# Performance work log

Measured on AMD Instinct MI355X. Metric: run time of the kernel, lower is better.

Reference implementation:

```python
import jax, jax.numpy as jnp
import numpy as np

N, H, K, T, B, IN_DIM, L = 1024, 64, 2, 12, 8, 2, 2
NNZ = 16384  # N * avg_degree(16)
M = 2 * K + 1  # supports_len * max_diffusion_step + 1 = 5


def setup_inputs() -> dict:
    key = jax.random.key(0)
    ks = jax.random.split(key, 13)

    def xavier(k, shape):
        std = 1.414 * (2.0 / (shape[0] + shape[1])) ** 0.5
        return std * jax.random.normal(k, shape, dtype=jnp.float32)

    F0 = IN_DIM + H  # 66
    F1 = 2 * H       # 128
    return {
        "inputs": jax.random.normal(ks[0], (T, B, N * IN_DIM), dtype=jnp.float32),
        "initial_hidden_state": jnp.zeros((L, B, N * H), dtype=jnp.float32),
        "support_rows": jax.random.randint(ks[1], (2, NNZ), 0, N, dtype=jnp.int32),
        "support_cols": jax.random.randint(ks[2], (2, NNZ), 0, N, dtype=jnp.int32),
        # scale like a random-walk-normalized adjacency (avg degree ~16)
        "support_vals": jax.random.uniform(ks[3], (2, NNZ), dtype=jnp.float32) / 16.0,
        "Wg0": xavier(ks[4], (F0 * M, 2 * H)),
        "bg0": 0.01 * jax.random.normal(ks[5], (2 * H,), dtype=jnp.float32),
        "Wc0": xavier(ks[6], (F0 * M, H)),
        "bc0": 0.01 * jax.random.normal(ks[7], (H,), dtype=jnp.float32),
        "Wg1": xavier(ks[8], (F1 * M, 2 * H)),
        "bg1": 0.01 * jax.random.normal(ks[9], (2 * H,), dtype=jnp.float32),
        "Wc1": xavier(ks[10], (F1 * M, H)),
        "bc1": 0.01 * jax.random.normal(ks[11], (H,), dtype=jnp.float32),
    }


def reference(inputs, initial_hidden_state, support_rows, support_cols, support_vals,
              Wg0, bg0, Wc0, bc0, Wg1, bg1, Wc1, bc1):
    supports = [(support_rows[i], support_cols[i], support_vals[i])
                for i in range(support_rows.shape[0])]

    def spmm(rows, cols, vals, x):  # sparse [N,N] @ x[N,FB]
        return jax.ops.segment_sum(vals[:, None] * x[cols], rows, num_segments=N)

    def diffuse(x):  # x: [B, N, F] -> [B*N, F*M] (Chebyshev-style recurrence)
        Bz, _, F = x.shape
        x0 = x.transpose(1, 2, 0).reshape(N, F * Bz)
        mats = [x0]
        for rows, cols, vals in supports:
            x1 = spmm(rows, cols, vals, x0)
            mats.append(x1)
            xkm2, xkm1 = x0, x1
            for _ in range(2, K + 1):
                xk = 2.0 * spmm(rows, cols, vals, xkm1) - xkm2
                mats.append(xk)
                xkm2, xkm1 = xkm1, xk
        Xs = jnp.stack(mats, 0).reshape(len(mats), N, F, Bz)
        return Xs.transpose(3, 1, 2, 0).reshape(Bz * N, F * len(mats))

    def cell(params, inp_t, state):  # one DCGRU step
        Wg, bg, Wc, bc = params
        Bz = inp_t.shape[0]
        xi = inp_t.reshape(Bz, N, -1)
        gates = jax.nn.sigmoid(
            diffuse(jnp.concatenate([xi, state.reshape(Bz, N, H)], 2)) @ Wg + bg
        ).reshape(Bz, N, 2 * H)
        r = gates[..., :H].reshape(Bz, N * H)
        u = gates[..., H:].reshape(Bz, N * H)
        cand_in = jnp.concatenate([xi, (r * state).reshape(Bz, N, H)], 2)
        c = jnp.tanh((diffuse(cand_in) @ Wc + bc).reshape(Bz, N * H))
        return u * state + (1.0 - u) * c

    layer_params = [(Wg0, bg0, Wc0, bc0), (Wg1, bg1, Wc1, bc1)]
    cur = inputs  # [T, B, N*input_dim]
    hiddens = []
    for l, params in enumerate(layer_params):
        def step(state, x_t, params=params):
            ns = cell(params, x_t, state)
            return ns, ns
        h_last, outs = jax.lax.scan(step, initial_hidden_state[l], cur)
        hiddens.append(h_last)
        cur = outs  # [T, B, N*H]
    return jnp.stack(hiddens, 0), cur
```

## Files before the change

### kernel.cpp

```cpp
#include <hip/hip_runtime.h>
#include <hip/hip_bf16.h>
#include <math.h>

#define NN 1024
#define HH 64
#define TT 12
#define BB 8
#define INDIM 2
#define LL 2
#define NNZE 16384
#define MM 5

#define FP0 96
#define FP1 128
#define CP0 (BB * FP0)
#define CP1 (BB * FP1)

static constexpr size_t BNH = (size_t)BB * NN * HH;

typedef short bf16x8 __attribute__((ext_vector_type(8)));
typedef float f32x4 __attribute__((ext_vector_type(4)));

__global__ void zero_int_kernel(int* p, int n) {
  int i = blockIdx.x * blockDim.x + threadIdx.x;
  if (i < n) p[i] = 0;
}

__global__ void copy_kernel(const float* __restrict__ src, float* __restrict__ dst, int n) {
  int i = blockIdx.x * blockDim.x + threadIdx.x;
  if (i < n) dst[i] = src[i];
}

__global__ void csr_count_kernel(const int* __restrict__ rows, int* __restrict__ counts) {
  int i = blockIdx.x * blockDim.x + threadIdx.x;
  if (i < 2 * NNZE) {
    int s = i / NNZE;
    atomicAdd(&counts[s * NN + rows[i]], 1);
  }
}

__global__ void csr_scan_kernel(const int* __restrict__ counts, int* __restrict__ row_start,
                                int* __restrict__ cursor) {
  __shared__ int bufA[NN];
  __shared__ int bufB[NN];
  int s = blockIdx.x;
  int t = threadIdx.x;
  bufA[t] = counts[s * NN + t];
  __syncthreads();
  int* src = bufA;
  int* dst = bufB;
  for (int off = 1; off < NN; off <<= 1) {
    dst[t] = src[t] + (t >= off ? src[t - off] : 0);
    __syncthreads();
    int* tmp = src; src = dst; dst = tmp;
  }
  row_start[s * (NN + 1) + t + 1] = src[t];
  cursor[s * NN + t] = (t == 0) ? 0 : src[t - 1];
  if (t == 0) row_start[s * (NN + 1)] = 0;
}

__global__ void csr_scatter_kernel(const int* __restrict__ rows, const int* __restrict__ colsIn,
                                   const float* __restrict__ valsIn, int* __restrict__ cursor,
                                   int* __restrict__ colsOut, float* __restrict__ valsOut) {
  int i = blockIdx.x * blockDim.x + threadIdx.x;
  if (i < 2 * NNZE) {
    int s = i / NNZE;
    int r = rows[i];
    int pos = atomicAdd(&cursor[s * NN + r], 1);
    colsOut[s * NNZE + pos] = colsIn[i];
    valsOut[s * NNZE + pos] = valsIn[i];
  }
}

__global__ void permwT_kernel(const float* __restrict__ W, unsigned short* __restrict__ WTh,
                              unsigned short* __restrict__ WTl, int F, int Fp, int J, int reord) {
  int Ktot = MM * Fp;
  int total = J * Ktot;
  for (int idx = blockIdx.x * blockDim.x + threadIdx.x; idx < total;
       idx += gridDim.x * blockDim.x) {
    int k = idx % Ktot;
    int j = idx / Ktot;
    int m = k / Fp;
    int fn = k - m * Fp;
    int fo;
    if (reord) {
      fo = (fn < HH) ? fn + INDIM : (fn < HH + INDIM ? fn - HH : -1);
    } else {
      fo = (fn < F) ? fn : -1;
    }
    float x = (fo >= 0) ? W[(size_t)(fo * MM + m) * J + j] : 0.f;
    unsigned u = __float_as_uint(x);
    unsigned short h = (unsigned short)(u >> 16);
    float hf = __uint_as_float(u & 0xFFFF0000u);
    WTh[idx] = h;
    WTl[idx] = (unsigned short)(__float_as_uint(x - hf) >> 16);
  }
}

template <int MODE>
__global__ __launch_bounds__(256) void spmm1_l1_kernel(
    const int* __restrict__ row_start, const int* __restrict__ cols,
    const float* __restrict__ vals, const float* __restrict__ xi,
    const float* __restrict__ state,
    const float* __restrict__ gates,
    float* __restrict__ mats) {
  const int r = blockIdx.x, s = blockIdx.y, tid = threadIdx.x;
  const int b = tid >> 5;
  const int f = (tid & 31) * 4;
  const bool isX = (f < HH);
  if (MODE && isX) return;
  const float* src = isX ? xi : state;
  const size_t srcBase = (size_t)b * NN * HH + (isX ? f : f - HH);
  const size_t gBase = (size_t)b * NN * (2 * HH) + (f - HH);

  const int* rs = row_start + s * (NN + 1);
  const int* cs = cols + s * NNZE;
  const float* vs = vals + s * NNZE;
  const int start = rs[r], end = rs[r + 1];

  float4 a0 = {0.f, 0.f, 0.f, 0.f}, a1 = {0.f, 0.f, 0.f, 0.f};
  int e = start;
  for (; e + 1 < end; e += 2) {
    int c0 = cs[e], c1 = cs[e + 1];
    float v0 = vs[e], v1 = vs[e + 1];
    float4 x0 = *(const float4*)(src + srcBase + (size_t)c0 * HH);
    float4 x1 = *(const float4*)(src + srcBase + (size_t)c1 * HH);
    if (MODE && !isX) {
      float4 g0 = *(const float4*)(gates + gBase + (size_t)c0 * (2 * HH));
      float4 g1 = *(const float4*)(gates + gBase + (size_t)c1 * (2 * HH));
      x0.x *= g0.x; x0.y *= g0.y; x0.z *= g0.z; x0.w *= g0.w;
      x1.x *= g1.x; x1.y *= g1.y; x1.z *= g1.z; x1.w *= g1.w;
    }
    a0.x += v0 * x0.x; a0.y += v0 * x0.y; a0.z += v0 * x0.z; a0.w += v0 * x0.w;
    a1.x += v1 * x1.x; a1.y += v1 * x1.y; a1.z += v1 * x1.z; a1.w += v1 * x1.w;
  }
  if (e < end) {
    int c0 = cs[e];
    float v0 = vs[e];
    float4 x0 = *(const float4*)(src + srcBase + (size_t)c0 * HH);
    if (MODE && !isX) {
      float4 g0 = *(const float4*)(gates + gBase + (size_t)c0 * (2 * HH));
      x0.x *= g0.x; x0.y *= g0.y; x0.z *= g0.z; x0.w *= g0.w;
    }
    a0.x += v0 * x0.x; a0.y += v0 * x0.y; a0.z += v0 * x0.z; a0.w += v0 * x0.w;
  }
  float4 o;
  o.x = a0.x + a1.x; o.y = a0.y + a1.y; o.z = a0.z + a1.z; o.w = a0.w + a1.w;
  *(float4*)(mats + (size_t)(1 + 2 * s) * (NN * CP1) + (size_t)r * CP1 + tid * 4) = o;

  if (s == 0) {
    float4 x = *(const float4*)(src + srcBase + (size_t)r * HH);
    if (MODE && !isX) {
      float4 g = *(const float4*)(gates + gBase + (size_t)r * (2 * HH));
      x.x *= g.x; x.y *= g.y; x.z *= g.z; x.w *= g.w;
    }
    *(float4*)(mats + (size_t)r * CP1 + tid * 4) = x;
  }
}

template <int MODE>
__global__ __launch_bounds__(256) void spmm1_l0_kernel(
    const int* __restrict__ row_start, const int* __restrict__ cols,
    const float* __restrict__ vals, const float* __restrict__ xi,
    const float* __restrict__ state,
    const float* __restrict__ gates,
    float* __restrict__ mats) {
  const int tid = threadIdx.x;
  constexpr int SLOTS = FP0 / 4;
  if (tid >= BB * SLOTS) return;
  const int r = blockIdx.x, s = blockIdx.y;
  const int b = tid / SLOTS;
  const int fn = (tid - b * SLOTS) * 4;
  const int c4 = b * FP0 + fn;

  float* x1p = mats + (size_t)(1 + 2 * s) * (NN * CP0) + (size_t)r * CP0 + c4;
  float* x0p = mats + (size_t)r * CP0 + c4;

  const int* rs = row_start + s * (NN + 1);
  const int* cs = cols + s * NNZE;
  const float* vs = vals + s * NNZE;
  const int start = rs[r], end = rs[r + 1];

  if (fn < HH) {
    const float* sb = state + (size_t)b * NN * HH + fn;
    const float* gb = gates + (size_t)b * NN * (2 * HH) + fn;
    float4 a0 = {0.f, 0.f, 0.f, 0.f}, a1 = {0.f, 0.f, 0.f, 0.f};
    int e = start;
    for (; e + 1 < end; e += 2) {
      int c0 = cs[e], c1 = cs[e + 1];
      float v0 = vs[e], v1 = vs[e + 1];
      float4 x0 = *(const float4*)(sb + (size_t)c0 * HH);
      float4 x1 = *(const float4*)(sb + (size_t)c1 * HH);
      if (MODE) {
        float4 g0 = *(const float4*)(gb + (size_t)c0 * (2 * HH));
        float4 g1 = *(const float4*)(gb + (size_t)c1 * (2 * HH));
        x0.x *= g0.x; x0.y *= g0.y; x0.z *= g0.z; x0.w *= g0.w;
        x1.x *= g1.x; x1.y *= g1.y; x1.z *= g1.z; x1.w *= g1.w;
      }
      a0.x += v0 * x0.x; a0.y += v0 * x0.y; a0.z += v0 * x0.z; a0.w += v0 * x0.w;
      a1.x += v1 * x1.x; a1.y += v1 * x1.y; a1.z += v1 * x1.z; a1.w += v1 * x1.w;
    }
    if (e < end) {
      int c0 = cs[e];
      float v0 = vs[e];
      float4 x0 = *(const float4*)(sb + (size_t)c0 * HH);
      if (MODE) {
        float4 g0 = *(const float4*)(gb + (size_t)c0 * (2 * HH));
        x0.x *= g0.x; x0.y *= g0.y; x0.z *= g0.z; x0.w *= g0.w;
      }
      a0.x += v0 * x0.x; a0.y += v0 * x0.y; a0.z += v0 * x0.z; a0.w += v0 * x0.w;
    }
    float4 o;
    o.x = a0.x + a1.x; o.y = a0.y + a1.y; o.z = a0.z + a1.z; o.w = a0.w + a1.w;
    *(float4*)x1p = o;
    if (s == 0) {
      float4 x = *(const float4*)(sb + (size_t)r * HH);
      if (MODE) {
        float4 g = *(const float4*)(gb + (size_t)r * (2 * HH));
        x.x *= g.x; x.y *= g.y; x.z *= g.z; x.w *= g.w;
      }
      *(float4*)x0p = x;
    }
  } else if (fn == HH) {
    if (MODE) return;
    const float* xb = xi + (size_t)b * NN * INDIM;
    float p0 = 0.f, p1 = 0.f, q0 = 0.f, q1 = 0.f;
    int e = start;
    for (; e + 1 < end; e += 2) {
      int c0 = cs[e], c1 = cs[e + 1];
      float v0 = vs[e], v1 = vs[e + 1];
      p0 += v0 * xb[(size_t)c0 * INDIM];
      q0 += v0 * xb[(size_t)c0 * INDIM + 1];
      p1 += v1 * xb[(size_t)c1 * INDIM];
      q1 += v1 * xb[(size_t)c1 * INDIM + 1];
    }
    if (e < end) {
      int c0 = cs[e];
      float v0 = vs[e];
      p0 += v0 * xb[(size_t)c0 * INDIM];
      q0 += v0 * xb[(size_t)c0 * INDIM + 1];
    }
    float4 o = {p0 + p1, q0 + q1, 0.f, 0.f};
    *(float4*)x1p = o;
    if (s == 0) {
      float4 x = {xb[(size_t)r * INDIM], xb[(size_t)r * INDIM + 1], 0.f, 0.f};
      *(float4*)x0p = x;
    }
  } else {
    if (MODE) return;
    float4 z = {0.f, 0.f, 0.f, 0.f};
    *(float4*)x1p = z;
    if (s == 0) *(float4*)x0p = z;
  }
}

template <int LAYER, int MODE>
__global__ __launch_bounds__(256) void spmm2_kernel(
    const int* __restrict__ row_start, const int* __restrict__ cols,
    const float* __restrict__ vals, float* __restrict__ mats) {
  constexpr int FPP = (LAYER == 0) ? FP0 : FP1;
  constexpr int CPX = BB * FPP;
  const int tid = threadIdx.x;
  int c4, fn;
  if (LAYER == 0) {
    constexpr int SLOTS = FP0 / 4;
    if (tid >= BB * SLOTS) return;
    const int b = tid / SLOTS;
    fn = (tid - b * SLOTS) * 4;
    c4 = b * FP0 + fn;
    if (MODE == 1 && fn >= HH) return;
  } else {
    c4 = tid * 4;
    fn = c4 & (FP1 - 1);
    if (MODE == 1 && fn < HH) return;
  }
  const int r = blockIdx.x, s = blockIdx.y;
  const size_t NC = (size_t)NN * CPX;
  float* xout = mats + (size_t)(2 + 2 * s) * NC + (size_t)r * CPX + c4;

  if (LAYER == 0 && MODE == 0 && fn >= HH + 4) {
    float4 z = {0.f, 0.f, 0.f, 0.f};
    *(float4*)xout = z;
    return;
  }

  const float* xin = mats + (size_t)(1 + 2 * s) * NC + c4;
  const int* rs = row_start + s * (NN + 1);
  const int* cs = cols + s * NNZE;
  const float* vs = vals + s * NNZE;
  const int start = rs[r], end = rs[r + 1];

  float4 a0 = {0.f, 0.f, 0.f, 0.f}, a1 = {0.f, 0.f, 0.f, 0.f};
  int e = start;
  for (; e + 1 < end; e += 2) {
    int c0 = cs[e], c1 = cs[e + 1];
    float v0 = vs[e], v1 = vs[e + 1];
    float4 x0 = *(const float4*)(xin + (size_t)c0 * CPX);
    float4 x1 = *(const float4*)(xin + (size_t)c1 * CPX);
    a0.x += v0 * x0.x; a0.y += v0 * x0.y; a0.z += v0 * x0.z; a0.w += v0 * x0.w;
    a1.x += v1 * x1.x; a1.y += v1 * x1.y; a1.z += v1 * x1.z; a1.w += v1 * x1.w;
  }
  if (e < end) {
    int c0 = cs[e];
    float v0 = vs[e];
    float4 x0 = *(const float4*)(xin + (size_t)c0 * CPX);
    a0.x += v0 * x0.x; a0.y += v0 * x0.y; a0.z += v0 * x0.z; a0.w += v0 * x0.w;
  }
  float4 p = *(const float4*)(mats + (size_t)r * CPX + c4);
  float4 o;
  o.x = 2.f * (a0.x + a1.x) - p.x;
  o.y = 2.f * (a0.y + a1.y) - p.y;
  o.z = 2.f * (a0.z + a1.z) - p.z;
  o.w = 2.f * (a0.w + a1.w) - p.w;
  *(float4*)xout = o;
}

template <int MODE, int FPP, int JJ>
__global__ __launch_bounds__(256) void gemm_mfma_kernel(
    const float* __restrict__ mats, const unsigned short* __restrict__ WTh,
    const unsigned short* __restrict__ WTl, const float* __restrict__ bias,
    float* __restrict__ gatesOut, const float* __restrict__ gatesIn,
    float* __restrict__ state, float* __restrict__ outT) {
  constexpr int KT = 32;
  constexpr int LDR = 56;
  constexpr int CP = BB * FPP;
  constexpr int KTOT = MM * FPP;
  constexpr int NPH = KTOT / KT;

  __shared__ unsigned short As[2][2][64][LDR];
  __shared__ unsigned short Ws[2][2][64][LDR];

  const int tid = threadIdx.x;
  const int lane = tid & 63;
  const int wid = tid >> 6;
  const int wr = wid >> 1, wc = wid & 1;
  const int lr = lane & 15, g = lane >> 4;

  const int bn0 = blockIdx.x * 64;
  const int jb0 = blockIdx.y * 64;
  const int nB = bn0 >> 10;
  const int n0 = bn0 & (NN - 1);

  const int srow = tid >> 2;
  const int scol = (tid & 3) * 8;

  float av[8];
  uint4 wh, wl;

  auto gload = [&](int ph) {
    const int m = (ph * KT) / FPP;
    const int f0 = (ph * KT) - m * FPP;
    const float* ab =
        mats + (size_t)m * NN * CP + (size_t)(n0 + srow) * CP + nB * FPP + f0 + scol;
    *(float4*)&av[0] = *(const float4*)ab;
    *(float4*)&av[4] = *(const float4*)(ab + 4);
    const size_t woff = (size_t)(jb0 + srow) * KTOT + ph * KT + scol;
    wh = *(const uint4*)(WTh + woff);
    wl = *(const uint4*)(WTl + woff);
  };
  auto stos = [&](int buf) {
    unsigned short h8[8], l8[8];
#pragma unroll
    for (int q = 0; q < 8; ++q) {
      float x = av[q];
      unsigned u = __float_as_uint(x);
      h8[q] = (unsigned short)(u >> 16);
      float hf = __uint_as_float(u & 0xFFFF0000u);
      l8[q] = (unsigned short)(__float_as_uint(x - hf) >> 16);
    }
    *(uint4*)&As[buf][0][srow][scol] = *(uint4*)h8;
    *(uint4*)&As[buf][1][srow][scol] = *(uint4*)l8;
    *(uint4*)&Ws[buf][0][srow][scol] = wh;
    *(uint4*)&Ws[buf][1][srow][scol] = wl;
  };

  f32x4 acc[2][2] = {};

  auto domfma = [&](int cur) {
    bf16x8 a[2][2], b[2][2];
#pragma unroll
    for (int tr = 0; tr < 2; ++tr)
#pragma unroll
      for (int pl = 0; pl < 2; ++pl)
        a[tr][pl] = *(const bf16x8*)&As[cur][pl][wr * 32 + tr * 16 + lr][g * 8];
#pragma unroll
    for (int tc = 0; tc < 2; ++tc)
#pragma unroll
      for (int pl = 0; pl < 2; ++pl)
        b[tc][pl] = *(const bf16x8*)&Ws[cur][pl][wc * 32 + tc * 16 + lr][g * 8];
#pragma unroll
    for (int tr = 0; tr < 2; ++tr)
#pragma unroll
      for (int tc = 0; tc < 2; ++tc) {
        acc[tr][tc] =
            __builtin_amdgcn_mfma_f32_16x16x32_bf16(a[tr][0], b[tc][0], acc[tr][tc], 0, 0, 0);
        acc[tr][tc] =
            __builtin_amdgcn_mfma_f32_16x16x32_bf16(a[tr][0], b[tc][1], acc[tr][tc], 0, 0, 0);
        acc[tr][tc] =
            __builtin_amdgcn_mfma_f32_16x16x32_bf16(a[tr][1], b[tc][0], acc[tr][tc], 0, 0, 0);
      }
  };

  gload(0);
  stos(0);
  __syncthreads();

  for (int ph = 0; ph < NPH; ++ph) {
    const int cur = ph & 1;
    if (ph + 1 < NPH) gload(ph + 1);
    domfma(cur);
    if (ph + 1 < NPH) {
      stos(cur ^ 1);
      __syncthreads();
    }
  }

#pragma unroll
  for (int tr = 0; tr < 2; ++tr)
#pragma unroll
    for (int tc = 0; tc < 2; ++tc) {
      const int jj = jb0 + wc * 32 + tc * 16 + lr;
      const float bs = bias[jj];
#pragma unroll
      for (int q = 0; q < 4; ++q) {
        const int bn = bn0 + wr * 32 + tr * 16 + g * 4 + q;
        float v = acc[tr][tc][q] + bs;
        if (MODE == 0) {
          gatesOut[(size_t)bn * (2 * HH) + jj] = 1.f / (1.f + expf(-v));
        } else {
          const int n = bn & (NN - 1);
          const int b = bn >> 10;
          float c = tanhf(v);
          float u = gatesIn[(size_t)bn * (2 * HH) + HH + jj];
          size_t si = (size_t)b * (NN * HH) + (size_t)n * HH + jj;
          float s = state[si];
          float ns = u * s + (1.f - u) * c;
          state[si] = ns;
          outT[si] = ns;
        }
      }
    }
}

extern "C" void kernel_launch(void* const* d_in, const int* in_sizes, int n_in, void* d_out,
                              int out_size, void* d_ws, size_t ws_size, hipStream_t stream) {
  const float* inputs = (const float*)d_in[0];
  const float* init_h = (const float*)d_in[1];
  const int* sup_rows = (const int*)d_in[2];
  const int* sup_cols = (const int*)d_in[3];
  const float* sup_vals = (const float*)d_in[4];
  const float* Wg[2] = {(const float*)d_in[5], (const float*)d_in[9]};
  const float* bg[2] = {(const float*)d_in[6], (const float*)d_in[10]};
  const float* Wc[2] = {(const float*)d_in[7], (const float*)d_in[11]};
  const float* bc[2] = {(const float*)d_in[8], (const float*)d_in[12]};

  float* out_h = (float*)d_out;
  float* out_cur = out_h + (size_t)LL * BNH;

  char* p = (char*)d_ws;
  auto alloc = [&](size_t bytes) -> void* {
    void* r = (void*)p;
    p += (bytes + 255) & ~(size_t)255;
    return r;
  };
  int* colsS = (int*)alloc(2 * NNZE * sizeof(int));
  float* valsS = (float*)alloc(2 * NNZE * sizeof(float));
  int* row_start = (int*)alloc(2 * (NN + 1) * sizeof(int));
  int* cursor = (int*)alloc(2 * NN * sizeof(int));
  int* counts = (int*)alloc(2 * NN * sizeof(int));
  const int K0 = MM * FP0, K1 = MM * FP1;
  unsigned short* WgTh[2];
  unsigned short* WgTl[2];
  unsigned short* WcTh[2];
  unsigned short* WcTl[2];
  WgTh[0] = (unsigned short*)alloc((size_t)128 * K0 * 2);
  WgTl[0] = (unsigned short*)alloc((size_t)128 * K0 * 2);
  WcTh[0] = (unsigned short*)alloc((size_t)64 * K0 * 2);
  WcTl[0] = (unsigned short*)alloc((size_t)64 * K0 * 2);
  WgTh[1] = (unsigned short*)alloc((size_t)128 * K1 * 2);
  WgTl[1] = (unsigned short*)alloc((size_t)128 * K1 * 2);
  WcTh[1] = (unsigned short*)alloc((size_t)64 * K1 * 2);
  WcTl[1] = (unsigned short*)alloc((size_t)64 * K1 * 2);
  float* mats = (float*)alloc((size_t)MM * NN * CP1 * sizeof(float));
  float* gatesBuf = (float*)alloc((size_t)BB * NN * 128 * sizeof(float));
  float* x01 = (float*)alloc(BNH * sizeof(float));

  zero_int_kernel<<<(2 * NN + 255) / 256, 256, 0, stream>>>(counts, 2 * NN);
  csr_count_kernel<<<(2 * NNZE + 255) / 256, 256, 0, stream>>>(sup_rows, counts);
  csr_scan_kernel<<<2, NN, 0, stream>>>(counts, row_start, cursor);
  csr_scatter_kernel<<<(2 * NNZE + 255) / 256, 256, 0, stream>>>(sup_rows, sup_cols, sup_vals,
                                                                 cursor, colsS, valsS);
  permwT_kernel<<<(128 * K0 + 255) / 256, 256, 0, stream>>>(Wg[0], WgTh[0], WgTl[0], 66, FP0, 128, 1);
  permwT_kernel<<<(64 * K0 + 255) / 256, 256, 0, stream>>>(Wc[0], WcTh[0], WcTl[0], 66, FP0, 64, 1);
  permwT_kernel<<<(128 * K1 + 255) / 256, 256, 0, stream>>>(Wg[1], WgTh[1], WgTl[1], 128, FP1, 128, 0);
  permwT_kernel<<<(64 * K1 + 255) / 256, 256, 0, stream>>>(Wc[1], WcTh[1], WcTl[1], 128, FP1, 64, 0);
  copy_kernel<<<((int)(LL * BNH) + 255) / 256, 256, 0, stream>>>(init_h, out_h, (int)(LL * BNH));

  for (int t = 0; t < TT; ++t) {
    {
      float* state = out_h;
      const float* xi = inputs + (size_t)t * BB * NN * INDIM;
      float* outT = x01;
      spmm1_l0_kernel<0><<<dim3(NN, 2), 256, 0, stream>>>(row_start, colsS, valsS, xi, state,
                                                          nullptr, mats);
      spmm2_kernel<0, 0><<<dim3(NN, 2), 256, 0, stream>>>(row_start, colsS, valsS, mats);
      gemm_mfma_kernel<0, FP0, 128><<<dim3(BB * NN / 64, 2), 256, 0, stream>>>(
          mats, WgTh[0], WgTl[0], bg[0], gatesBuf, nullptr, nullptr, nullptr);
      spmm1_l0_kernel<1><<<dim3(NN, 2), 256, 0, stream>>>(row_start, colsS, valsS, xi, state,
                                                          gatesBuf, mats);
      spmm2_kernel<0, 1><<<dim3(NN, 2), 256, 0, stream>>>(row_start, colsS, valsS, mats);
      gemm_mfma_kernel<1, FP0, 64><<<dim3(BB * NN / 64, 1), 256, 0, stream>>>(
          mats, WcTh[0], WcTl[0], bc[0], nullptr, gatesBuf, state, outT);
    }
    {
      float* state = out_h + BNH;
      const float* xi = x01;
      float* outT = out_cur + (size_t)t * BNH;
      spmm1_l1_kernel<0><<<dim3(NN, 2), 256, 0, stream>>>(row_start, colsS, valsS, xi, state,
                                                          nullptr, mats);
      spmm2_kernel<1, 0><<<dim3(NN, 2), 256, 0, stream>>>(row_start, colsS, valsS, mats);
      gemm_mfma_kernel<0, FP1, 128><<<dim3(BB * NN / 64, 2), 256, 0, stream>>>(
          mats, WgTh[1], WgTl[1], bg[1], gatesBuf, nullptr, nullptr, nullptr);
      spmm1_l1_kernel<1><<<dim3(NN, 2), 256, 0, stream>>>(row_start, colsS, valsS, xi, state,
                                                          gatesBuf, mats);
      spmm2_kernel<1, 1><<<dim3(NN, 2), 256, 0, stream>>>(row_start, colsS, valsS, mats);
      gemm_mfma_kernel<1, FP1, 64><<<dim3(BB * NN / 64, 1), 256, 0, stream>>>(
          mats, WcTh[1], WcTl[1], bc[1], nullptr, gatesBuf, state, outT);
    }
  }
}
```

Before: 2.037 ms.

## Add dedicated state-only SpMM kernels, unroll SpMM by four, halve GEMM row tile

Adds dedicated spmm1/spmm2 state kernels for the candidate pass. They pack two rows per 256-thread block, so no threads return idle as they did in the old MODE=1 variants. All SpMM loops are unrolled to four independent accumulators for more memory-level parallelism. The GEMM gets a BM template parameter and now launches with 32-row tiles, doubling the grid for better occupancy across CUs at the cost of less weight reuse per block.

Result: faster. 1.877 ms (-7.8%).

```diff
diff --git a/kernel.cpp b/kernel.cpp
--- a/kernel.cpp
+++ b/kernel.cpp
@@ -20,6 +20,16 @@
 
 typedef short bf16x8 __attribute__((ext_vector_type(8)));
 typedef float f32x4 __attribute__((ext_vector_type(4)));
+
+__device__ __forceinline__ void fma4(float4& acc, float v, const float4& p) {
+  acc.x += v * p.x;
+  acc.y += v * p.y;
+  acc.z += v * p.z;
+  acc.w += v * p.w;
+}
+__device__ __forceinline__ void mul4(float4& a, const float4& g) {
+  a.x *= g.x; a.y *= g.y; a.z *= g.z; a.w *= g.w;
+}
 
 __global__ void zero_int_kernel(int* p, int n) {
   int i = blockIdx.x * blockDim.x + threadIdx.x;
@@ -90,80 +100,62 @@
     }
     float x = (fo >= 0) ? W[(size_t)(fo * MM + m) * J + j] : 0.f;
     unsigned u = __float_as_uint(x);
-    unsigned short h = (unsigned short)(u >> 16);
+    WTh[idx] = (unsigned short)(u >> 16);
     float hf = __uint_as_float(u & 0xFFFF0000u);
-    WTh[idx] = h;
     WTl[idx] = (unsigned short)(__float_as_uint(x - hf) >> 16);
   }
 }
 
-template <int MODE>
 __global__ __launch_bounds__(256) void spmm1_l1_kernel(
     const int* __restrict__ row_start, const int* __restrict__ cols,
     const float* __restrict__ vals, const float* __restrict__ xi,
     const float* __restrict__ state,
-    const float* __restrict__ gates,
     float* __restrict__ mats) {
   const int r = blockIdx.x, s = blockIdx.y, tid = threadIdx.x;
   const int b = tid >> 5;
   const int f = (tid & 31) * 4;
   const bool isX = (f < HH);
-  if (MODE && isX) return;
   const float* src = isX ? xi : state;
-  const size_t srcBase = (size_t)b * NN * HH + (isX ? f : f - HH);
-  const size_t gBase = (size_t)b * NN * (2 * HH) + (f - HH);
+  const float* sb = src + (size_t)b * NN * HH + (isX ? f : f - HH);
 
   const int* rs = row_start + s * (NN + 1);
   const int* cs = cols + s * NNZE;
   const float* vs = vals + s * NNZE;
   const int start = rs[r], end = rs[r + 1];
 
-  float4 a0 = {0.f, 0.f, 0.f, 0.f}, a1 = {0.f, 0.f, 0.f, 0.f};
+  float4 a0 = {0, 0, 0, 0}, a1 = {0, 0, 0, 0}, a2 = {0, 0, 0, 0}, a3 = {0, 0, 0, 0};
   int e = start;
-  for (; e + 1 < end; e += 2) {
-    int c0 = cs[e], c1 = cs[e + 1];
-    float v0 = vs[e], v1 = vs[e + 1];
-    float4 x0 = *(const float4*)(src + srcBase + (size_t)c0 * HH);
-    float4 x1 = *(const float4*)(src + srcBase + (size_t)c1 * HH);
-    if (MODE && !isX) {
-      float4 g0 = *(const float4*)(gates + gBase + (size_t)c0 * (2 * HH));
-      float4 g1 = *(const float4*)(gates + gBase + (size_t)c1 * (2 * HH));
-      x0.x *= g0.x; x0.y *= g0.y; x0.z *= g0.z; x0.w *= g0.w;
-      x1.x *= g1.x; x1.y *= g1.y; x1.z *= g1.z; x1.w *= g1.w;
-    }
-    a0.x += v0 * x0.x; a0.y += v0 * x0.y; a0.z += v0 * x0.z; a0.w += v0 * x0.w;
-    a1.x += v1 * x1.x; a1.y += v1 * x1.y; a1.z += v1 * x1.z; a1.w += v1 * x1.w;
-  }
-  if (e < end) {
+  for (; e + 3 < end; e += 4) {
+    int c0 = cs[e], c1 = cs[e + 1], c2 = cs[e + 2], c3 = cs[e + 3];
+    float v0 = vs[e], v1 = vs[e + 1], v2 = vs[e + 2], v3 = vs[e + 3];
+    float4 x0 = *(const float4*)(sb + (size_t)c0 * HH);
+    float4 x1 = *(const float4*)(sb + (size_t)c1 * HH);
+    float4 x2 = *(const float4*)(sb + (size_t)c2 * HH);
+    float4 x3 = *(const float4*)(sb + (size_t)c3 * HH);
+    fma4(a0, v0, x0); fma4(a1, v1, x1); fma4(a2, v2, x2); fma4(a3, v3, x3);
+  }
+  for (; e < end; ++e) {
     int c0 = cs[e];
     float v0 = vs[e];
-    float4 x0 = *(const float4*)(src + srcBase + (size_t)c0 * HH);
-    if (MODE && !isX) {
-      float4 g0 = *(const float4*)(gates + gBase + (size_t)c0 * (2 * HH));
-      x0.x *= g0.x; x0.y *= g0.y; x0.z *= g0.z; x0.w *= g0.w;
-    }
-    a0.x += v0 * x0.x; a0.y += v0 * x0.y; a0.z += v0 * x0.z; a0.w += v0 * x0.w;
+    float4 x0 = *(const float4*)(sb + (size_t)c0 * HH);
+    fma4(a0, v0, x0);
   }
   float4 o;
-  o.x = a0.x + a1.x; o.y = a0.y + a1.y; o.z = a0.z + a1.z; o.w = a0.w + a1.w;
+  o.x = (a0.x + a1.x) + (a2.x + a3.x);
+  o.y = (a0.y + a1.y) + (a2.y + a3.y);
+  o.z = (a0.z + a1.z) + (a2.z + a3.z);
+  o.w = (a0.w + a1.w) + (a2.w + a3.w);
   *(float4*)(mats + (size_t)(1 + 2 * s) * (NN * CP1) + (size_t)r * CP1 + tid * 4) = o;
 
   if (s == 0) {
-    float4 x = *(const float4*)(src + srcBase + (size_t)r * HH);
-    if (MODE && !isX) {
-      float4 g = *(const float4*)(gates + gBase + (size_t)r * (2 * HH));
-      x.x *= g.x; x.y *= g.y; x.z *= g.z; x.w *= g.w;
-    }
-    *(float4*)(mats + (size_t)r * CP1 + tid * 4) = x;
-  }
-}
-
-template <int MODE>
+    *(float4*)(mats + (size_t)r * CP1 + tid * 4) = *(const float4*)(sb + (size_t)r * HH);
+  }
+}
+
 __global__ __launch_bounds__(256) void spmm1_l0_kernel(
     const int* __restrict__ row_start, const int* __restrict__ cols,
     const float* __restrict__ vals, const float* __restrict__ xi,
     const float* __restrict__ state,
-    const float* __restrict__ gates,
     float* __restrict__ mats) {
   const int tid = threadIdx.x;
   constexpr int SLOTS = FP0 / 4;
@@ -183,46 +175,31 @@
 
   if (fn < HH) {
     const float* sb = state + (size_t)b * NN * HH + fn;
-    const float* gb = gates + (size_t)b * NN * (2 * HH) + fn;
-    float4 a0 = {0.f, 0.f, 0.f, 0.f}, a1 = {0.f, 0.f, 0.f, 0.f};
+    float4 a0 = {0, 0, 0, 0}, a1 = {0, 0, 0, 0}, a2 = {0, 0, 0, 0}, a3 = {0, 0, 0, 0};
     int e = start;
-    for (; e + 1 < end; e += 2) {
-      int c0 = cs[e], c1 = cs[e + 1];
-      float v0 = vs[e], v1 = vs[e + 1];
+    for (; e + 3 < end; e += 4) {
+      int c0 = cs[e], c1 = cs[e + 1], c2 = cs[e + 2], c3 = cs[e + 3];
+      float v0 = vs[e], v1 = vs[e + 1], v2 = vs[e + 2], v3 = vs[e + 3];
       float4 x0 = *(const float4*)(sb + (size_t)c0 * HH);
       float4 x1 = *(const float4*)(sb + (size_t)c1 * HH);
-      if (MODE) {
-        float4 g0 = *(const float4*)(gb + (size_t)c0 * (2 * HH));
-        float4 g1 = *(const float4*)(gb + (size_t)c1 * (2 * HH));
-        x0.x *= g0.x; x0.y *= g0.y; x0.z *= g0.z; x0.w *= g0.w;
-        x1.x *= g1.x; x1.y *= g1.y; x1.z *= g1.z; x1.w *= g1.w;
-      }
-      a0.x += v0 * x0.x; a0.y += v0 * x0.y; a0.z += v0 * x0.z; a0.w += v0 * x0.w;
-      a1.x += v1 * x1.x; a1.y += v1 * x1.y; a1.z += v1 * x1.z; a1.w += v1 * x1.w;
-    }
-    if (e < end) {
+      float4 x2 = *(const float4*)(sb + (size_t)c2 * HH);
+      float4 x3 = *(const float4*)(sb + (size_t)c3 * HH);
+      fma4(a0, v0, x0); fma4(a1, v1, x1); fma4(a2, v2, x2); fma4(a3, v3, x3);
+    }
+    for (; e < end; ++e) {
       int c0 = cs[e];
       float v0 = vs[e];
       float4 x0 = *(const float4*)(sb + (size_t)c0 * HH);
-      if (MODE) {
-        float4 g0 = *(const float4*)(gb + (size_t)c0 * (2 * HH));
-        x0.x *= g0.x; x0.y *= g0.y; x0.z *= g0.z; x0.w *= g0.w;
-      }
-      a0.x += v0 * x0.x; a0.y += v0 * x0.y; a0.z += v0 * x0.z; a0.w += v0 * x0.w;
+      fma4(a0, v0, x0);
     }
     float4 o;
-    o.x = a0.x + a1.x; o.y = a0.y + a1.y; o.z = a0.z + a1.z; o.w = a0.w + a1.w;
+    o.x = (a0.x + a1.x) + (a2.x + a3.x);
+    o.y = (a0.y + a1.y) + (a2.y + a3.y);
+    o.z = (a0.z + a1.z) + (a2.z + a3.z);
+    o.w = (a0.w + a1.w) + (a2.w + a3.w);
     *(float4*)x1p = o;
-    if (s == 0) {
-      float4 x = *(const float4*)(sb + (size_t)r * HH);
-      if (MODE) {
-        float4 g = *(const float4*)(gb + (size_t)r * (2 * HH));
-        x.x *= g.x; x.y *= g.y; x.z *= g.z; x.w *= g.w;
-      }
-      *(float4*)x0p = x;
-    }
+    if (s == 0) *(float4*)x0p = *(const float4*)(sb + (size_t)r * HH);
   } else if (fn == HH) {
-    if (MODE) return;
     const float* xb = xi + (size_t)b * NN * INDIM;
     float p0 = 0.f, p1 = 0.f, q0 = 0.f, q1 = 0.f;
     int e = start;
@@ -247,14 +224,76 @@
       *(float4*)x0p = x;
     }
   } else {
-    if (MODE) return;
-    float4 z = {0.f, 0.f, 0.f, 0.f};
+    float4 z = {0, 0, 0, 0};
     *(float4*)x1p = z;
     if (s == 0) *(float4*)x0p = z;
   }
 }
 
-template <int LAYER, int MODE>
+template <int LAYER>
+__global__ __launch_bounds__(256) void spmm1_state_kernel(
+    const int* __restrict__ row_start, const int* __restrict__ cols,
+    const float* __restrict__ vals, const float* __restrict__ state,
+    const float* __restrict__ gates, float* __restrict__ mats) {
+  constexpr int FPP = (LAYER == 0) ? FP0 : FP1;
+  constexpr int CP = BB * FPP;
+  constexpr int BASE = (LAYER == 0) ? 0 : HH;
+  const int tid = threadIdx.x;
+  const int r = blockIdx.x * 2 + (tid >> 7);
+  const int slot = tid & 127;
+  const int b = slot >> 4;
+  const int fi = (slot & 15) * 4;
+  const int s = blockIdx.y;
+
+  const float* sb = state + (size_t)b * NN * HH + fi;
+  const float* gb = gates + (size_t)b * NN * (2 * HH) + fi;
+
+  const int* rs = row_start + s * (NN + 1);
+  const int* cs = cols + s * NNZE;
+  const float* vs = vals + s * NNZE;
+  const int start = rs[r], end = rs[r + 1];
+
+  float4 a0 = {0, 0, 0, 0}, a1 = {0, 0, 0, 0}, a2 = {0, 0, 0, 0}, a3 = {0, 0, 0, 0};
+  int e = start;
+  for (; e + 3 < end; e += 4) {
+    int c0 = cs[e], c1 = cs[e + 1], c2 = cs[e + 2], c3 = cs[e + 3];
+    float v0 = vs[e], v1 = vs[e + 1], v2 = vs[e + 2], v3 = vs[e + 3];
+    float4 x0 = *(const float4*)(sb + (size_t)c0 * HH);
+    float4 g0 = *(const float4*)(gb + (size_t)c0 * (2 * HH));
+    float4 x1 = *(const float4*)(sb + (size_t)c1 * HH);
+    float4 g1 = *(const float4*)(gb + (size_t)c1 * (2 * HH));
+    float4 x2 = *(const float4*)(sb + (size_t)c2 * HH);
+    float4 g2 = *(const float4*)(gb + (size_t)c2 * (2 * HH));
+    float4 x3 = *(const float4*)(sb + (size_t)c3 * HH);
+    float4 g3 = *(const float4*)(gb + (size_t)c3 * (2 * HH));
+    mul4(x0, g0); mul4(x1, g1); mul4(x2, g2); mul4(x3, g3);
+    fma4(a0, v0, x0); fma4(a1, v1, x1); fma4(a2, v2, x2); fma4(a3, v3, x3);
+  }
+  for (; e < end; ++e) {
+    int c0 = cs[e];
+    float v0 = vs[e];
+    float4 x0 = *(const float4*)(sb + (size_t)c0 * HH);
+    float4 g0 = *(const float4*)(gb + (size_t)c0 * (2 * HH));
+    mul4(x0, g0);
+    fma4(a0, v0, x0);
+  }
+  float4 o;
+  o.x = (a0.x + a1.x) + (a2.x + a3.x);
+  o.y = (a0.y + a1.y) + (a2.y + a3.y);
+  o.z = (a0.z + a1.z) + (a2.z + a3.z);
+  o.w = (a0.w + a1.w) + (a2.w + a3.w);
+  const int c4 = b * FPP + BASE + fi;
+  *(float4*)(mats + (size_t)(1 + 2 * s) * (NN * CP) + (size_t)r * CP + c4) = o;
+
+  if (s == 0) {
+    float4 x = *(const float4*)(sb + (size_t)r * HH);
+    float4 g = *(const float4*)(gb + (size_t)r * (2 * HH));
+    mul4(x, g);
+    *(float4*)(mats + (size_t)r * CP + c4) = x;
+  }
+}
+
+template <int LAYER>
 __global__ __launch_bounds__(256) void spmm2_kernel(
     const int* __restrict__ row_start, const int* __restrict__ cols,
     const float* __restrict__ vals, float* __restrict__ mats) {
@@ -268,18 +307,16 @@
     const int b = tid / SLOTS;
     fn = (tid - b * SLOTS) * 4;
     c4 = b * FP0 + fn;
-    if (MODE == 1 && fn >= HH) return;
   } else {
     c4 = tid * 4;
     fn = c4 & (FP1 - 1);
-    if (MODE == 1 && fn < HH) return;
   }
   const int r = blockIdx.x, s = blockIdx.y;
   const size_t NC = (size_t)NN * CPX;
   float* xout = mats + (size_t)(2 + 2 * s) * NC + (size_t)r * CPX + c4;
 
-  if (LAYER == 0 && MODE == 0 && fn >= HH + 4) {
-    float4 z = {0.f, 0.f, 0.f, 0.f};
+  if (LAYER == 0 && fn >= HH + 4) {
+    float4 z = {0, 0, 0, 0};
     *(float4*)xout = z;
     return;
   }
@@ -290,32 +327,81 @@
   const float* vs = vals + s * NNZE;
   const int start = rs[r], end = rs[r + 1];
 
-  float4 a0 = {0.f, 0.f, 0.f, 0.f}, a1 = {0.f, 0.f, 0.f, 0.f};
+  float4 a0 = {0, 0, 0, 0}, a1 = {0, 0, 0, 0}, a2 = {0, 0, 0, 0}, a3 = {0, 0, 0, 0};
   int e = start;
-  for (; e + 1 < end; e += 2) {
-    int c0 = cs[e], c1 = cs[e + 1];
-    float v0 = vs[e], v1 = vs[e + 1];
+  for (; e + 3 < end; e += 4) {
+    int c0 = cs[e], c1 = cs[e + 1], c2 = cs[e + 2], c3 = cs[e + 3];
+    float v0 = vs[e], v1 = vs[e + 1], v2 = vs[e + 2], v3 = vs[e + 3];
     float4 x0 = *(const float4*)(xin + (size_t)c0 * CPX);
     float4 x1 = *(const float4*)(xin + (size_t)c1 * CPX);
-    a0.x += v0 * x0.x; a0.y += v0 * x0.y; a0.z += v0 * x0.z; a0.w += v0 * x0.w;
-    a1.x += v1 * x1.x; a1.y += v1 * x1.y; a1.z += v1 * x1.z; a1.w += v1 * x1.w;
-  }
-  if (e < end) {
+    float4 x2 = *(const float4*)(xin + (size_t)c2 * CPX);
+    float4 x3 = *(const float4*)(xin + (size_t)c3 * CPX);
+    fma4(a0, v0, x0); fma4(a1, v1, x1); fma4(a2, v2, x2); fma4(a3, v3, x3);
+  }
+  for (; e < end; ++e) {
     int c0 = cs[e];
     float v0 = vs[e];
     float4 x0 = *(const float4*)(xin + (size_t)c0 * CPX);
-    a0.x += v0 * x0.x; a0.y += v0 * x0.y; a0.z += v0 * x0.z; a0.w += v0 * x0.w;
+    fma4(a0, v0, x0);
   }
   float4 p = *(const float4*)(mats + (size_t)r * CPX + c4);
   float4 o;
-  o.x = 2.f * (a0.x + a1.x) - p.x;
-  o.y = 2.f * (a0.y + a1.y) - p.y;
-  o.z = 2.f * (a0.z + a1.z) - p.z;
-  o.w = 2.f * (a0.w + a1.w) - p.w;
+  o.x = 2.f * ((a0.x + a1.x) + (a2.x + a3.x)) - p.x;
+  o.y = 2.f * ((a0.y + a1.y) + (a2.y + a3.y)) - p.y;
+  o.z = 2.f * ((a0.z + a1.z) + (a2.z + a3.z)) - p.z;
+  o.w = 2.f * ((a0.w + a1.w) + (a2.w + a3.w)) - p.w;
   *(float4*)xout = o;
 }
 
-template <int MODE, int FPP, int JJ>
+template <int LAYER>
+__global__ __launch_bounds__(256) void spmm2_state_kernel(
+    const int* __restrict__ row_start, const int* __restrict__ cols,
+    const float* __restrict__ vals, float* __restrict__ mats) {
+  constexpr int FPP = (LAYER == 0) ? FP0 : FP1;
+  constexpr int CP = BB * FPP;
+  constexpr int BASE = (LAYER == 0) ? 0 : HH;
+  const int tid = threadIdx.x;
+  const int r = blockIdx.x * 2 + (tid >> 7);
+  const int slot = tid & 127;
+  const int b = slot >> 4;
+  const int fi = (slot & 15) * 4;
+  const int s = blockIdx.y;
+  const int c4 = b * FPP + BASE + fi;
+  const size_t NC = (size_t)NN * CP;
+
+  const float* xin = mats + (size_t)(1 + 2 * s) * NC + c4;
+  const int* rs = row_start + s * (NN + 1);
+  const int* cs = cols + s * NNZE;
+  const float* vs = vals + s * NNZE;
+  const int start = rs[r], end = rs[r + 1];
+
+  float4 a0 = {0, 0, 0, 0}, a1 = {0, 0, 0, 0}, a2 = {0, 0, 0, 0}, a3 = {0, 0, 0, 0};
+  int e = start;
+  for (; e + 3 < end; e += 4) {
+    int c0 = cs[e], c1 = cs[e + 1], c2 = cs[e + 2], c3 = cs[e + 3];
+    float v0 = vs[e], v1 = vs[e + 1], v2 = vs[e + 2], v3 = vs[e + 3];
+    float4 x0 = *(const float4*)(xin + (size_t)c0 * CP);
+    float4 x1 = *(const float4*)(xin + (size_t)c1 * CP);
+    float4 x2 = *(const float4*)(xin + (size_t)c2 * CP);
+    float4 x3 = *(const float4*)(xin + (size_t)c3 * CP);
+    fma4(a0, v0, x0); fma4(a1, v1, x1); fma4(a2, v2, x2); fma4(a3, v3, x3);
+  }
+  for (; e < end; ++e) {
+    int c0 = cs[e];
+    float v0 = vs[e];
+    float4 x0 = *(const float4*)(xin + (size_t)c0 * CP);
+    fma4(a0, v0, x0);
+  }
+  float4 p = *(const float4*)(mats + (size_t)r * CP + c4);
+  float4 o;
+  o.x = 2.f * ((a0.x + a1.x) + (a2.x + a3.x)) - p.x;
+  o.y = 2.f * ((a0.y + a1.y) + (a2.y + a3.y)) - p.y;
+  o.z = 2.f * ((a0.z + a1.z) + (a2.z + a3.z)) - p.z;
+  o.w = 2.f * ((a0.w + a1.w) + (a2.w + a3.w)) - p.w;
+  *(float4*)(mats + (size_t)(2 + 2 * s) * NC + (size_t)r * CP + c4) = o;
+}
+
+template <int MODE, int BM, int FPP, int JJ>
 __global__ __launch_bounds__(256) void gemm_mfma_kernel(
     const float* __restrict__ mats, const unsigned short* __restrict__ WTh,
     const unsigned short* __restrict__ WTl, const float* __restrict__ bias,
@@ -326,23 +412,26 @@
   constexpr int CP = BB * FPP;
   constexpr int KTOT = MM * FPP;
   constexpr int NPH = KTOT / KT;
-
-  __shared__ unsigned short As[2][2][64][LDR];
+  constexpr int WTC = (BM == 64) ? 2 : 1;
+
+  __shared__ unsigned short As[2][2][BM][LDR];
   __shared__ unsigned short Ws[2][2][64][LDR];
 
   const int tid = threadIdx.x;
   const int lane = tid & 63;
   const int wid = tid >> 6;
-  const int wr = wid >> 1, wc = wid & 1;
+  const int wr = (BM == 64) ? (wid >> 1) * 32 : 0;
+  const int wc = (BM == 64) ? (wid & 1) * 32 : wid * 16;
   const int lr = lane & 15, g = lane >> 4;
 
-  const int bn0 = blockIdx.x * 64;
+  const int bn0 = blockIdx.x * BM;
   const int jb0 = blockIdx.y * 64;
   const int nB = bn0 >> 10;
   const int n0 = bn0 & (NN - 1);
 
   const int srow = tid >> 2;
   const int scol = (tid & 3) * 8;
+  const bool doA = (BM == 64) || (tid < 128);
 
   float av[8];
   uint4 wh, wl;
@@ -350,48 +439,52 @@
   auto gload = [&](int ph) {
     const int m = (ph * KT) / FPP;
     const int f0 = (ph * KT) - m * FPP;
-    const float* ab =
-        mats + (size_t)m * NN * CP + (size_t)(n0 + srow) * CP + nB * FPP + f0 + scol;
-    *(float4*)&av[0] = *(const float4*)ab;
-    *(float4*)&av[4] = *(const float4*)(ab + 4);
+    if (doA) {
+      const float* ab =
+          mats + (size_t)m * NN * CP + (size_t)(n0 + srow) * CP + nB * FPP + f0 + scol;
+      *(float4*)&av[0] = *(const float4*)ab;
+      *(float4*)&av[4] = *(const float4*)(ab + 4);
+    }
     const size_t woff = (size_t)(jb0 + srow) * KTOT + ph * KT + scol;
     wh = *(const uint4*)(WTh + woff);
     wl = *(const uint4*)(WTl + woff);
   };
   auto stos = [&](int buf) {
-    unsigned short h8[8], l8[8];
-#pragma unroll
-    for (int q = 0; q < 8; ++q) {
-      float x = av[q];
-      unsigned u = __float_as_uint(x);
-      h8[q] = (unsigned short)(u >> 16);
-      float hf = __uint_as_float(u & 0xFFFF0000u);
-      l8[q] = (unsigned short)(__float_as_uint(x - hf) >> 16);
-    }
-    *(uint4*)&As[buf][0][srow][scol] = *(uint4*)h8;
-    *(uint4*)&As[buf][1][srow][scol] = *(uint4*)l8;
+    if (doA) {
+      unsigned short h8[8], l8[8];
+#pragma unroll
+      for (int q = 0; q < 8; ++q) {
+        float x = av[q];
+        unsigned u = __float_as_uint(x);
+        h8[q] = (unsigned short)(u >> 16);
+        float hf = __uint_as_float(u & 0xFFFF0000u);
+        l8[q] = (unsigned short)(__float_as_uint(x - hf) >> 16);
+      }
+      *(uint4*)&As[buf][0][srow][scol] = *(uint4*)h8;
+      *(uint4*)&As[buf][1][srow][scol] = *(uint4*)l8;
+    }
     *(uint4*)&Ws[buf][0][srow][scol] = wh;
     *(uint4*)&Ws[buf][1][srow][scol] = wl;
   };
 
-  f32x4 acc[2][2] = {};
+  f32x4 acc[2][WTC] = {};
 
   auto domfma = [&](int cur) {
-    bf16x8 a[2][2], b[2][2];
+    bf16x8 a[2][2], b[WTC][2];
 #pragma unroll
     for (int tr = 0; tr < 2; ++tr)
 #pragma unroll
       for (int pl = 0; pl < 2; ++pl)
-        a[tr][pl] = *(const bf16x8*)&As[cur][pl][wr * 32 + tr * 16 + lr][g * 8];
-#pragma unroll
-    for (int tc = 0; tc < 2; ++tc)
+        a[tr][pl] = *(const bf16x8*)&As[cur][pl][wr + tr * 16 + lr][g * 8];
+#pragma unroll
+    for (int tc = 0; tc < WTC; ++tc)
 #pragma unroll
       for (int pl = 0; pl < 2; ++pl)
-        b[tc][pl] = *(const bf16x8*)&Ws[cur][pl][wc * 32 + tc * 16 + lr][g * 8];
+        b[tc][pl] = *(const bf16x8*)&Ws[cur][pl][wc + tc * 16 + lr][g * 8];
 #pragma unroll
     for (int tr = 0; tr < 2; ++tr)
 #pragma unroll
-      for (int tc = 0; tc < 2; ++tc) {
+      for (int tc = 0; tc < WTC; ++tc) {
         acc[tr][tc] =
             __builtin_amdgcn_mfma_f32_16x16x32_bf16(a[tr][0], b[tc][0], acc[tr][tc], 0, 0, 0);
         acc[tr][tc] =
@@ -418,12 +511,12 @@
 #pragma unroll
   for (int tr = 0; tr < 2; ++tr)
 #pragma unroll
-    for (int tc = 0; tc < 2; ++tc) {
-      const int jj = jb0 + wc * 32 + tc * 16 + lr;
+    for (int tc = 0; tc < WTC; ++tc) {
+      const int jj = jb0 + wc + tc * 16 + lr;
       const float bs = bias[jj];
 #pragma unroll
       for (int q = 0; q < 4; ++q) {
-        const int bn = bn0 + wr * 32 + tr * 16 + g * 4 + q;
+        const int bn = bn0 + wr + tr * 16 + g * 4 + q;
         float v = acc[tr][tc][q] + bs;
         if (MODE == 0) {
           gatesOut[(size_t)bn * (2 * HH) + jj] = 1.f / (1.f + expf(-v));
@@ -501,30 +594,28 @@
       float* state = out_h;
       const float* xi = inputs + (size_t)t * BB * NN * INDIM;
       float* outT = x01;
-      spmm1_l0_kernel<0><<<dim3(NN, 2), 256, 0, stream>>>(row_start, colsS, valsS, xi, state,
-                                                          nullptr, mats);
-      spmm2_kernel<0, 0><<<dim3(NN, 2), 256, 0, stream>>>(row_start, colsS, valsS, mats);
-      gemm_mfma_kernel<0, FP0, 128><<<dim3(BB * NN / 64, 2), 256, 0, stream>>>(
+      spmm1_l0_kernel<<<dim3(NN, 2), 256, 0, stream>>>(row_start, colsS, valsS, xi, state, mats);
+      spmm2_kernel<0><<<dim3(NN, 2), 256, 0, stream>>>(row_start, colsS, valsS, mats);
+      gemm_mfma_kernel<0, 32, FP0, 128><<<dim3(BB * NN / 32, 2), 256, 0, stream>>>(
           mats, WgTh[0], WgTl[0], bg[0], gatesBuf, nullptr, nullptr, nullptr);
-      spmm1_l0_kernel<1><<<dim3(NN, 2), 256, 0, stream>>>(row_start, colsS, valsS, xi, state,
-                                                          gatesBuf, mats);
-      spmm2_kernel<0, 1><<<dim3(NN, 2), 256, 0, stream>>>(row_start, colsS, valsS, mats);
-      gemm_mfma_kernel<1, FP0, 64><<<dim3(BB * NN / 64, 1), 256, 0, stream>>>(
+      spmm1_state_kernel<0><<<dim3(NN / 2, 2), 256, 0, stream>>>(row_start, colsS, valsS, state,
+                                                                 gatesBuf, mats);
+      spmm2_state_kernel<0><<<dim3(NN / 2, 2), 256, 0, stream>>>(row_start, colsS, valsS, mats);
+      gemm_mfma_kernel<1, 32, FP0, 64><<<dim3(BB * NN / 32, 1), 256, 0, stream>>>(
           mats, WcTh[0], WcTl[0], bc[0], nullptr, gatesBuf, state, outT);
     }
     {
       float* state = out_h + BNH;
       const float* xi = x01;
       float* outT = out_cur + (size_t)t * BNH;
-      spmm1_l1_kernel<0><<<dim3(NN, 2), 256, 0, stream>>>(row_start, colsS, valsS, xi, state,
-                                                          nullptr, mats);
-      spmm2_kernel<1, 0><<<dim3(NN, 2), 256, 0, stream>>>(row_start, colsS, valsS, mats);
-      gemm_mfma_kernel<0, FP1, 128><<<dim3(BB * NN / 64, 2), 256, 0, stream>>>(
+      spmm1_l1_kernel<<<dim3(NN, 2), 256, 0, stream>>>(row_start, colsS, valsS, xi, state, mats);
+      spmm2_kernel<1><<<dim3(NN, 2), 256, 0, stream>>>(row_start, colsS, valsS, mats);
+      gemm_mfma_kernel<0, 32, FP1, 128><<<dim3(BB * NN / 32, 2), 256, 0, stream>>>(
           mats, WgTh[1], WgTl[1], bg[1], gatesBuf, nullptr, nullptr, nullptr);
-      spmm1_l1_kernel<1><<<dim3(NN, 2), 256, 0, stream>>>(row_start, colsS, valsS, xi, state,
-                                                          gatesBuf, mats);
-      spmm2_kernel<1, 1><<<dim3(NN, 2), 256, 0, stream>>>(row_start, colsS, valsS, mats);
-      gemm_mfma_kernel<1, FP1, 64><<<dim3(BB * NN / 64, 1), 256, 0, stream>>>(
+      spmm1_state_kernel<1><<<dim3(NN / 2, 2), 256, 0, stream>>>(row_start, colsS, valsS, state,
+                                                                 gatesBuf, mats);
+      spmm2_state_kernel<1><<<dim3(NN / 2, 2), 256, 0, stream>>>(row_start, colsS, valsS, mats);
+      gemm_mfma_kernel<1, 32, FP1, 64><<<dim3(BB * NN / 32, 1), 256, 0, stream>>>(
           mats, WcTh[1], WcTl[1], bc[1], nullptr, gatesBuf, state, outT);
     }
   }
```
